# Optimization experiments

Hardware: AMD Instinct MI355X
Metric: run time of the kernel (lower is better)

## Reference

```python
import jax, jax.numpy as jnp
import numpy as np

B, S, D, H, V, N_SHARDS, CAP = 4, 512, 512, 8, 32000, 64, 128
HD = D // H


def _layernorm(x, g, b, eps=1e-5):
    mu = x.mean(-1, keepdims=True)
    var = ((x - mu) ** 2).mean(-1, keepdims=True)
    return (x - mu) * jax.lax.rsqrt(var + eps) * g + b


def setup_inputs() -> dict:
    key = jax.random.key(0)
    ks = jax.random.split(key, 16)
    s = 0.02
    return {
        'input_ids': jax.random.randint(ks[0], (B, S), 0, V, dtype=jnp.int32),
        'emb': jax.random.normal(ks[1], (V, D), jnp.float32) * s,
        'Wq': jax.random.normal(ks[2], (D, D), jnp.float32) * s,
        'Wk': jax.random.normal(ks[3], (D, D), jnp.float32) * s,
        'Wv': jax.random.normal(ks[4], (D, D), jnp.float32) * s,
        'Wo': jax.random.normal(ks[5], (D, D), jnp.float32) * s,
        'ln_g': jnp.ones((D,), jnp.float32),
        'ln_b': jnp.zeros((D,), jnp.float32),
        'W_router': jax.random.normal(ks[6], (D, N_SHARDS), jnp.float32),
        'mem_keys': jax.random.normal(ks[7], (N_SHARDS, CAP, D), jnp.float32) * s,
        'mem_values': jax.random.normal(ks[8], (N_SHARDS, CAP, D), jnp.float32) * s,
        'Wg_c': jax.random.normal(ks[9], (D, D), jnp.float32) * s,
        'Wg_m': jax.random.normal(ks[10], (D, D), jnp.float32) * s,
        'bg': jnp.zeros((D,), jnp.float32),
        'Wd': jax.random.normal(ks[11], (D, V), jnp.float32) * s,
        'bd': jnp.zeros((V,), jnp.float32),
        'top_k': 4,
    }


def reference(input_ids, emb, Wq, Wk, Wv, Wo, ln_g, ln_b, W_router,
              mem_keys, mem_values, Wg_c, Wg_m, bg, Wd, bd, top_k):
    # --- encode_context: embedding + causal MHA block (ContextSynthesizer) ---
    x = emb[input_ids]                                   # [B,S,D]
    q = (x @ Wq).reshape(B, S, H, HD)
    k = (x @ Wk).reshape(B, S, H, HD)
    v = (x @ Wv).reshape(B, S, H, HD)
    att = jnp.einsum('bqhd,bkhd->bhqk', q, k) / jnp.sqrt(jnp.float32(HD))
    causal = jnp.tril(jnp.ones((S, S), bool))
    att = jnp.where(causal[None, None], att, jnp.finfo(att.dtype).min)
    att = jax.nn.softmax(att, axis=-1)
    o = jnp.einsum('bhqk,bkhd->bqhd', att, v).reshape(B, S, D) @ Wo
    ctx = _layernorm(x + o, ln_g, ln_b)                  # [B,S,D]

    # --- LSHRouter: hyperplane projection -> shard id per token ---
    routes = jnp.argmax(ctx @ W_router, axis=-1)         # [B,S] int

    # --- MemoryShardStore.query, batched: per-token routed shard top-k read ---
    keys_g = mem_keys[routes]                            # [B,S,CAP,D] irregular gather
    scores = jnp.einsum('bscd,bsd->bsc', keys_g, ctx)    # [B,S,CAP]
    top_v, top_i = jax.lax.top_k(scores, top_k)          # [B,S,k]
    w = jax.nn.softmax(top_v, axis=-1)
    vals = mem_values[routes[:, :, None], top_i]         # [B,S,k,D]
    memory_stream = jnp.einsum('bsk,bskd->bsd', w, vals)

    # --- GatedMemoryFusion ---
    gate = jax.nn.sigmoid(ctx @ Wg_c + memory_stream @ Wg_m + bg)
    fused = gate * ctx + (1.0 - gate) * memory_stream

    # --- decoder; payload bias is zero (store holds no sequence_chunk records) ---
    logits = fused @ Wd + bd                             # [B,S,V]
    return logits
```

## Files before the change

kernel.cpp:

```cpp
#include <hip/hip_runtime.h>

typedef unsigned short u16;
typedef float f32x4 __attribute__((ext_vector_type(4)));
typedef short short8 __attribute__((ext_vector_type(8)));
typedef __bf16 bf16x8 __attribute__((ext_vector_type(8)));

#define B_  4
#define S_  512
#define D_  512
#define H_  8
#define HD_ 64
#define V_  32000
#define NSHARD_ 64
#define CAP_ 128
#define TOK_ (B_ * S_)

__device__ __forceinline__ float bf2f(u16 u) { return __uint_as_float(((unsigned)u) << 16); }
__device__ __forceinline__ u16 f2bf(float f) {
  unsigned u = __float_as_uint(f);
  u += 0x7FFFu + ((u >> 16) & 1u);
  return (u16)(u >> 16);
}

__device__ __forceinline__ f32x4 mfma16(short8 a, short8 b, f32x4 c) {
  return __builtin_amdgcn_mfma_f32_16x16x32_bf16(
      __builtin_bit_cast(bf16x8, a), __builtin_bit_cast(bf16x8, b), c, 0, 0, 0);
}

__device__ __forceinline__ void load_lds16(const void* g, void* l) {
  __builtin_amdgcn_global_load_lds(
      (const __attribute__((address_space(1))) void*)g,
      (__attribute__((address_space(3))) void*)l, 16, 0, 0);
}

template<int NS, bool ACC, int OM, bool CKLIM>
__global__ __launch_bounds__(256) void gemm_bt(
    const u16* __restrict__ Ah, const u16* __restrict__ Al, int ldA, long sA1, long sA2,
    const u16* __restrict__ Bh, const u16* __restrict__ Bl, int ldB, long sB1, long sB2,
    void* __restrict__ C0, void* __restrict__ C1, int ldC, long sC1, long sC2,
    int K, int z2n, float alpha)
{
  __shared__ u16 AsH[64 * 64];
  __shared__ u16 BsH[64 * 64];
  __shared__ u16 AsL[(NS == 3) ? 64 * 64 : 8];
  __shared__ u16 BsL[(NS == 3) ? 64 * 64 : 8];

  const int n0 = blockIdx.x * 64;
  const int m0 = blockIdx.y * 64;

  const int z = blockIdx.z;
  const int z1 = z / z2n, z2 = z - z1 * z2n;
  const long baseA = (long)z1 * sA1 + (long)z2 * sA2;
  const long baseB = (long)z1 * sB1 + (long)z2 * sB2;
  const long baseC = (long)z1 * sC1 + (long)z2 * sC2;

  const int tid = threadIdx.x;
  const int lane = tid & 63;
  const int w = tid >> 6;
  const int wm = (w >> 1) * 32, wn = (w & 1) * 32;
  const int fr = lane & 15, kg = lane >> 4;

  const int srow = lane >> 3;
  const int schunk = (lane & 7) ^ srow;

  const u16* gAh = Ah + baseA + (long)(m0 + w * 16 + srow) * ldA + schunk * 8;
  const u16* gBh = Bh + baseB + (long)(n0 + w * 16 + srow) * ldB + schunk * 8;
  const u16* gAl = (NS == 3) ? (Al + baseA + (long)(m0 + w * 16 + srow) * ldA + schunk * 8) : nullptr;
  const u16* gBl = (NS == 3) ? (Bl + baseB + (long)(n0 + w * 16 + srow) * ldB + schunk * 8) : nullptr;
  u16* lAh = &AsH[(w * 16) * 64];
  u16* lBh = &BsH[(w * 16) * 64];
  u16* lAl = &AsL[(NS == 3) ? (w * 16) * 64 : 0];
  u16* lBl = &BsL[(NS == 3) ? (w * 16) * 64 : 0];

  const int kmax = CKLIM ? (m0 + 64) : K;

  f32x4 acc[2][2] = {};

  for (int k0 = 0; k0 < kmax; k0 += 64) {
    load_lds16(gAh + k0, lAh);
    load_lds16(gAh + k0 + 8 * ldA, lAh + 8 * 64);
    load_lds16(gBh + k0, lBh);
    load_lds16(gBh + k0 + 8 * ldB, lBh + 8 * 64);
    if (NS == 3) {
      load_lds16(gAl + k0, lAl);
      load_lds16(gAl + k0 + 8 * ldA, lAl + 8 * 64);
      load_lds16(gBl + k0, lBl);
      load_lds16(gBl + k0 + 8 * ldB, lBl + 8 * 64);
    }
    __syncthreads();

    short8 ah[2][2], bh[2][2], al[2][2], bl[2][2];
#pragma unroll
    for (int mi = 0; mi < 2; ++mi) {
      int row = wm + mi * 16 + fr;
#pragma unroll
      for (int ks = 0; ks < 2; ++ks) {
        int idx = row * 64 + ((ks * 32 + kg * 8) ^ ((fr & 7) << 3));
        ah[mi][ks] = *(const short8*)&AsH[idx];
        if (NS == 3) al[mi][ks] = *(const short8*)&AsL[idx];
      }
    }
#pragma unroll
    for (int ni = 0; ni < 2; ++ni) {
      int row = wn + ni * 16 + fr;
#pragma unroll
      for (int ks = 0; ks < 2; ++ks) {
        int idx = row * 64 + ((ks * 32 + kg * 8) ^ ((fr & 7) << 3));
        bh[ni][ks] = *(const short8*)&BsH[idx];
        if (NS == 3) bl[ni][ks] = *(const short8*)&BsL[idx];
      }
    }
#pragma unroll
    for (int ks = 0; ks < 2; ++ks)
#pragma unroll
      for (int mi = 0; mi < 2; ++mi)
#pragma unroll
        for (int ni = 0; ni < 2; ++ni) {
          acc[mi][ni] = mfma16(ah[mi][ks], bh[ni][ks], acc[mi][ni]);
          if (NS == 3) {
            acc[mi][ni] = mfma16(ah[mi][ks], bl[ni][ks], acc[mi][ni]);
            acc[mi][ni] = mfma16(al[mi][ks], bh[ni][ks], acc[mi][ni]);
          }
        }
    __syncthreads();
  }

#pragma unroll
  for (int mi = 0; mi < 2; ++mi)
#pragma unroll
    for (int ni = 0; ni < 2; ++ni) {
      int gnc = n0 + wn + ni * 16 + fr;
#pragma unroll
      for (int r = 0; r < 4; ++r) {
        int gm = m0 + wm + mi * 16 + kg * 4 + r;
        float v = acc[mi][ni][r] * alpha;
        long idx = baseC + (long)gm * ldC + gnc;
        if (OM == 0) {
          float* C = (float*)C0;
          C[idx] = ACC ? (C[idx] + v) : v;
        } else {
          u16 h = f2bf(v);
          ((u16*)C0)[idx] = h;
          ((u16*)C1)[idx] = f2bf(v - bf2f(h));
        }
      }
    }
}

__global__ __launch_bounds__(256) void gate_gemm_k(
    const u16* __restrict__ Ah, const u16* __restrict__ Bh,
    const float* __restrict__ bgp, const float* __restrict__ ctxf,
    const float* __restrict__ msf, u16* __restrict__ fused)
{
  __shared__ u16 AsH[64 * 64];
  __shared__ u16 BsH[64 * 64];

  const int n0 = blockIdx.x * 64;
  const int m0 = blockIdx.y * 64;
  const int tid = threadIdx.x;
  const int lane = tid & 63;
  const int w = tid >> 6;
  const int wm = (w >> 1) * 32, wn = (w & 1) * 32;
  const int fr = lane & 15, kg = lane >> 4;
  const int srow = lane >> 3;
  const int schunk = (lane & 7) ^ srow;

  const u16* gAh = Ah + (long)(m0 + w * 16 + srow) * 1024 + schunk * 8;
  const u16* gBh = Bh + (long)(n0 + w * 16 + srow) * 1024 + schunk * 8;
  u16* lAh = &AsH[(w * 16) * 64];
  u16* lBh = &BsH[(w * 16) * 64];

  f32x4 acc[2][2] = {};

  for (int k0 = 0; k0 < 1024; k0 += 64) {
    load_lds16(gAh + k0, lAh);
    load_lds16(gAh + k0 + 8 * 1024, lAh + 8 * 64);
    load_lds16(gBh + k0, lBh);
    load_lds16(gBh + k0 + 8 * 1024, lBh + 8 * 64);
    __syncthreads();

    short8 ah[2][2], bh[2][2];
#pragma unroll
    for (int mi = 0; mi < 2; ++mi) {
      int row = wm + mi * 16 + fr;
#pragma unroll
      for (int ks = 0; ks < 2; ++ks)
        ah[mi][ks] = *(const short8*)&AsH[row * 64 +
                         ((ks * 32 + kg * 8) ^ ((fr & 7) << 3))];
    }
#pragma unroll
    for (int ni = 0; ni < 2; ++ni) {
      int row = wn + ni * 16 + fr;
#pragma unroll
      for (int ks = 0; ks < 2; ++ks)
        bh[ni][ks] = *(const short8*)&BsH[row * 64 +
                         ((ks * 32 + kg * 8) ^ ((fr & 7) << 3))];
    }
#pragma unroll
    for (int ks = 0; ks < 2; ++ks)
#pragma unroll
      for (int mi = 0; mi < 2; ++mi)
#pragma unroll
        for (int ni = 0; ni < 2; ++ni)
          acc[mi][ni] = mfma16(ah[mi][ks], bh[ni][ks], acc[mi][ni]);
    __syncthreads();
  }

#pragma unroll
  for (int mi = 0; mi < 2; ++mi)
#pragma unroll
    for (int ni = 0; ni < 2; ++ni) {
      int gnc = n0 + wn + ni * 16 + fr;
      float bv = bgp[gnc];
#pragma unroll
      for (int r = 0; r < 4; ++r) {
        int gm = m0 + wm + mi * 16 + kg * 4 + r;
        long idx = (long)gm * D_ + gnc;
        float g = 1.f / (1.f + expf(-(acc[mi][ni][r] + bv)));
        fused[idx] = f2bf(g * ctxf[idx] + (1.f - g) * msf[idx]);
      }
    }
}

__global__ __launch_bounds__(256) void qkt_k(
    const u16* __restrict__ qkvh, const u16* __restrict__ qkvl,
    float* __restrict__ att)
{
  const int n0 = blockIdx.x * 64;
  const int m0 = blockIdx.y * 64;
  if (n0 > m0 + 63) return;
  const int z = blockIdx.z;
  const int b = z >> 3, h = z & 7;
  const long qbase = (long)b * 512 * 1536 + h * 64;
  const long kbase = qbase + 512;
  const long cbase = (long)z * 512 * 512;

  const int tid = threadIdx.x;
  const int lane = tid & 63;
  const int w = tid >> 6;
  const int wm = (w >> 1) * 32, wn = (w & 1) * 32;
  const int fr = lane & 15, kg = lane >> 4;

  short8 ah[2][2], al[2][2], bh[2][2], bl[2][2];
#pragma unroll
  for (int mi = 0; mi < 2; ++mi)
#pragma unroll
    for (int ks = 0; ks < 2; ++ks) {
      long ra = qbase + (long)(m0 + wm + mi * 16 + fr) * 1536 + ks * 32 + kg * 8;
      ah[mi][ks] = *(const short8*)(qkvh + ra);
      al[mi][ks] = *(const short8*)(qkvl + ra);
    }
#pragma unroll
  for (int ni = 0; ni < 2; ++ni)
#pragma unroll
    for (int ks = 0; ks < 2; ++ks) {
      long rb = kbase + (long)(n0 + wn + ni * 16 + fr) * 1536 + ks * 32 + kg * 8;
      bh[ni][ks] = *(const short8*)(qkvh + rb);
      bl[ni][ks] = *(const short8*)(qkvl + rb);
    }

  f32x4 acc[2][2] = {};
#pragma unroll
  for (int ks = 0; ks < 2; ++ks)
#pragma unroll
    for (int mi = 0; mi < 2; ++mi)
#pragma unroll
      for (int ni = 0; ni < 2; ++ni) {
        acc[mi][ni] = mfma16(ah[mi][ks], bh[ni][ks], acc[mi][ni]);
        acc[mi][ni] = mfma16(ah[mi][ks], bl[ni][ks], acc[mi][ni]);
        acc[mi][ni] = mfma16(al[mi][ks], bh[ni][ks], acc[mi][ni]);
      }

#pragma unroll
  for (int mi = 0; mi < 2; ++mi)
#pragma unroll
    for (int ni = 0; ni < 2; ++ni) {
      int gnc = n0 + wn + ni * 16 + fr;
#pragma unroll
      for (int r = 0; r < 4; ++r) {
        int gm = m0 + wm + mi * 16 + kg * 4 + r;
        att[cbase + (long)gm * 512 + gnc] = acc[mi][ni][r] * 0.125f;
      }
    }
}

__global__ __launch_bounds__(512, 4) void logits_gemm_bk32_k(
    const u16* __restrict__ A, const u16* __restrict__ Bt,
    const float* __restrict__ bias, float* __restrict__ C)
{
  __shared__ u16 As[2][256 * 32];
  __shared__ u16 Bs[2][128 * 32];

  const int id = blockIdx.x;
  const int swz = (id & 7) * 250 + (id >> 3);
  const int m0 = (swz & 7) * 256;
  const int n0 = (swz >> 3) * 128;

  const int tid = threadIdx.x;
  const int lane = tid & 63;
  const int wid = tid >> 6;
  const int wr = wid >> 1;
  const int wc = wid & 1;
  const int fr = lane & 15, kg = lane >> 4;
  const int srow = lane >> 2;
  const int schunk = (lane & 3) ^ (srow & 3);

  f32x4 acc[4][4] = {};
  short8 a[4], b[4];

  auto stage = [&](int kt) {
    const int buf = kt & 1;
    const long kc = (long)kt * 32 + schunk * 8;
    load_lds16(A + (long)(m0 + wid * 16 + srow) * D_ + kc,
               &As[buf][(wid * 16) * 32]);
    load_lds16(A + (long)(m0 + 128 + wid * 16 + srow) * D_ + kc,
               &As[buf][(128 + wid * 16) * 32]);
    load_lds16(Bt + (long)(n0 + wid * 16 + srow) * D_ + kc,
               &Bs[buf][(wid * 16) * 32]);
  };
  auto readfrags = [&](int buf) {
#pragma unroll
    for (int mi = 0; mi < 4; ++mi) {
      int row = wr * 64 + mi * 16 + fr;
      a[mi] = *(const short8*)&As[buf][row * 32 + ((kg ^ (row & 3)) * 8)];
    }
#pragma unroll
    for (int ni = 0; ni < 4; ++ni) {
      int row = wc * 64 + ni * 16 + fr;
      b[ni] = *(const short8*)&Bs[buf][row * 32 + ((kg ^ (row & 3)) * 8)];
    }
  };

  stage(0);
  stage(1);

  for (int t = 0; t < 16; ++t) {
    __builtin_amdgcn_sched_barrier(0);
    if (t < 15) { asm volatile("s_waitcnt vmcnt(3)" ::: "memory"); }
    else        { asm volatile("s_waitcnt vmcnt(0)" ::: "memory"); }
    __builtin_amdgcn_s_barrier();
    __builtin_amdgcn_sched_barrier(0);

    readfrags(t & 1);
    asm volatile("s_waitcnt lgkmcnt(0)" ::: "memory");
    __builtin_amdgcn_sched_barrier(0);
    __builtin_amdgcn_s_barrier();
    __builtin_amdgcn_sched_barrier(0);

    if (t + 2 < 16) stage(t + 2);

    __builtin_amdgcn_sched_barrier(0);
    __builtin_amdgcn_s_setprio(1);
#pragma unroll
    for (int mi = 0; mi < 4; ++mi)
#pragma unroll
      for (int ni = 0; ni < 4; ++ni)
        acc[mi][ni] = mfma16(a[mi], b[ni], acc[mi][ni]);
    __builtin_amdgcn_s_setprio(0);
    __builtin_amdgcn_sched_barrier(0);
  }

#pragma unroll
  for (int ni = 0; ni < 4; ++ni) {
    int gnc = n0 + wc * 64 + ni * 16 + fr;
    float bv = bias[gnc];
#pragma unroll
    for (int mi = 0; mi < 4; ++mi)
#pragma unroll
      for (int r = 0; r < 4; ++r) {
        int gm = m0 + wr * 64 + mi * 16 + kg * 4 + r;
        __builtin_nontemporal_store(acc[mi][ni][r] + bv, &C[(long)gm * V_ + gnc]);
      }
  }
}

__global__ __launch_bounds__(256) void prep_weights_k(
    const float* __restrict__ Wq, const float* __restrict__ Wk,
    const float* __restrict__ Wv, const float* __restrict__ Wo,
    const float* __restrict__ Wgc, const float* __restrict__ Wgm,
    const float* __restrict__ Wd,
    u16* __restrict__ wqkvTh, u16* __restrict__ wqkvTl,
    u16* __restrict__ woTh, u16* __restrict__ woTl,
    u16* __restrict__ wgT, u16* __restrict__ wdT)
{
  const int bid = blockIdx.x;
  const float* W; u16 *oh, *ol = nullptr;
  int ldw, ldo, koff = 0, nb, kb;
  bool LO = false;
  if (bid < 384) {
    const int w = bid >> 6, tt = bid & 63;
    nb = tt & 7; kb = tt >> 3;
    ldw = 512; ldo = 512;
    switch (w) {
      case 0: W = Wq;  oh = wqkvTh;               ol = wqkvTl;               LO = true; break;
      case 1: W = Wk;  oh = wqkvTh + 512 * 512;   ol = wqkvTl + 512 * 512;   LO = true; break;
      case 2: W = Wv;  oh = wqkvTh + 2 * 512 * 512; ol = wqkvTl + 2 * 512 * 512; LO = true; break;
      case 3: W = Wo;  oh = woTh;                 ol = woTl;                 LO = true; break;
      case 4: W = Wgc; oh = wgT; ldo = 1024; break;
      default: W = Wgm; oh = wgT; ldo = 1024; koff = 512; break;
    }
  } else {
    const int tt = bid - 384;
    nb = tt % 500; kb = tt / 500;
    W = Wd; ldw = V_; ldo = 512; oh = wdT;
  }
  const int n0 = nb * 64, k0 = kb * 64;
  const int tid = threadIdx.x;
  __shared__ float t[64][65];
  {
    const int kk = tid >> 4;
    const int c4 = (tid & 15) * 4;
#pragma unroll
    for (int i = 0; i < 4; ++i) {
      f32x4 v = *(const f32x4*)(W + (long)(k0 + kk + i * 16) * ldw + n0 + c4);
      t[kk + i * 16][c4] = v[0];
      t[kk + i * 16][c4 + 1] = v[1];
      t[kk + i * 16][c4 + 2] = v[2];
      t[kk + i * 16][c4 + 3] = v[3];
    }
  }
  __syncthreads();
  {
    const int chunk = tid & 7;
    const int nn = tid >> 3;
#pragma unroll
    for (int j = 0; j < 2; ++j) {
      int n = nn + j * 32;
      u16 hbuf[8], lbuf[8];
#pragma unroll
      for (int e = 0; e < 8; ++e) {
        float fv = t[chunk * 8 + e][n];
        u16 h = f2bf(fv);
        hbuf[e] = h;
        lbuf[e] = f2bf(fv - bf2f(h));
      }
      long ob = (long)(n0 + n) * ldo + koff + k0 + chunk * 8;
      *(short8*)(oh + ob) = *(short8*)hbuf;
      if (LO) *(short8*)(ol + ob) = *(short8*)lbuf;
    }
  }
}

__global__ __launch_bounds__(256) void v_transpose_k(
    const u16* __restrict__ qh, const u16* __restrict__ ql,
    u16* __restrict__ vTh, u16* __restrict__ vTl)
{
  __shared__ u16 th[64][68];
  __shared__ u16 tl[64][68];
  const int z = blockIdx.y;
  const int b = z >> 3, h = z & 7;
  const int s0 = blockIdx.x * 64;
  const long ibase = ((long)(b * 512 + s0)) * 1536 + 1024 + h * 64;
  const int tid = threadIdx.x;
  {
    const int sr = tid >> 2;
    const int c8 = (tid & 3) * 16;
    const long src = ibase + (long)sr * 1536 + c8;
    *(short8*)&th[sr][c8]     = *(const short8*)(qh + src);
    *(short8*)&th[sr][c8 + 8] = *(const short8*)(qh + src + 8);
    *(short8*)&tl[sr][c8]     = *(const short8*)(ql + src);
    *(short8*)&tl[sr][c8 + 8] = *(const short8*)(ql + src + 8);
  }
  __syncthreads();
  {
    const int dr = tid >> 2;
    const int s8 = (tid & 3) * 16;
    u16 oh[16], ol[16];
#pragma unroll
    for (int j = 0; j < 16; ++j) { oh[j] = th[s8 + j][dr]; ol[j] = tl[s8 + j][dr]; }
    long ob = (long)z * 64 * 512 + (long)dr * 512 + s0 + s8;
    *(short8*)(vTh + ob)     = *(short8*)&oh[0];
    *(short8*)(vTh + ob + 8) = *(short8*)&oh[8];
    *(short8*)(vTl + ob)     = *(short8*)&ol[0];
    *(short8*)(vTl + ob + 8) = *(short8*)&ol[8];
  }
}

__global__ __launch_bounds__(128) void embed_k(const int* __restrict__ ids,
                                               const float* __restrict__ emb,
                                               float* __restrict__ x,
                                               u16* __restrict__ xh,
                                               u16* __restrict__ xl) {
  const int t = blockIdx.x;
  const long id = ids[t];
  const int c = threadIdx.x * 4;
  f32x4 v = *(const f32x4*)(emb + id * (long)D_ + c);
  *(f32x4*)(x + (long)t * D_ + c) = v;
  u16 hh[4], ll[4];
#pragma unroll
  for (int j = 0; j < 4; ++j) {
    u16 h = f2bf(v[j]);
    hh[j] = h;
    ll[j] = f2bf(v[j] - bf2f(h));
  }
  *(unsigned long long*)(xh + (long)t * D_ + c) = *(unsigned long long*)hh;
  *(unsigned long long*)(xl + (long)t * D_ + c) = *(unsigned long long*)ll;
}

__global__ __launch_bounds__(64) void softmax_causal_k(
    const float* __restrict__ att, u16* __restrict__ ph, u16* __restrict__ pl) {
  const int row = blockIdx.x;
  const int i = row & 511;
  const long base = (long)row << 9;
  const float* p = att + base;
  const int lane = threadIdx.x;
  const int c0 = lane * 8;
  float v[8];
  float m = -3.4e38f;
  if (c0 <= i) {
    f32x4 a = *(const f32x4*)(p + c0);
    f32x4 b2 = *(const f32x4*)(p + c0 + 4);
#pragma unroll
    for (int j = 0; j < 8; ++j) {
      float x = (j < 4) ? a[j] : b2[j - 4];
      x = (c0 + j <= i) ? x : -3.4e38f;
      v[j] = x;
      m = fmaxf(m, x);
    }
  } else {
#pragma unroll
    for (int j = 0; j < 8; ++j) v[j] = 0.f;
  }
#pragma unroll
  for (int off = 32; off; off >>= 1) m = fmaxf(m, __shfl_xor(m, off));
  float s = 0.f;
  if (c0 <= i) {
#pragma unroll
    for (int j = 0; j < 8; ++j) {
      float e = (c0 + j <= i) ? expf(v[j] - m) : 0.f;
      v[j] = e;
      s += e;
    }
  }
#pragma unroll
  for (int off = 32; off; off >>= 1) s += __shfl_xor(s, off);
  float inv = 1.f / s;
  if (c0 <= (i | 63)) {
    u16 hh[8], ll[8];
#pragma unroll
    for (int j = 0; j < 8; ++j) {
      float e = (c0 <= i) ? v[j] * inv : 0.f;
      u16 h = f2bf(e);
      hh[j] = h;
      ll[j] = f2bf(e - bf2f(h));
    }
    *(short8*)(ph + base + c0) = *(short8*)hh;
    *(short8*)(pl + base + c0) = *(short8*)ll;
  }
}

__global__ __launch_bounds__(128) void ln_route_k(
    const float* __restrict__ x, const float* __restrict__ proj,
    const float* __restrict__ g, const float* __restrict__ b,
    const float* __restrict__ Wr, const float* __restrict__ keys,
    const float* __restrict__ valsm,
    float* __restrict__ ctxf, u16* __restrict__ catA, float* __restrict__ msf)
{
  const int t = blockIdx.x;
  const int tid = threadIdx.x;
  __shared__ float sctx[D_];
  __shared__ float red2[4];
  __shared__ float spart[CAP_];
  __shared__ float sred2[2][64];
  __shared__ int s_route;
  __shared__ int sidx[4];
  __shared__ float sw[4];

  const int c = tid * 4;
  f32x4 xv = *(const f32x4*)(x + (long)t * D_ + c);
  f32x4 pv = *(const f32x4*)(proj + (long)t * D_ + c);
  float v0 = xv[0] + pv[0], v1 = xv[1] + pv[1];
  float v2 = xv[2] + pv[2], v3 = xv[3] + pv[3];
  float s = v0 + v1 + v2 + v3;
  float q = v0 * v0 + v1 * v1 + v2 * v2 + v3 * v3;
#pragma unroll
  for (int off = 32; off; off >>= 1) { s += __shfl_xor(s, off); q += __shfl_xor(q, off); }
  const int wave = tid >> 6, lane = tid & 63;
  if (lane == 0) { red2[wave] = s; red2[2 + wave] = q; }
  __syncthreads();
  s = red2[0] + red2[1];
  q = red2[2] + red2[3];
  float mu = s * (1.f / 512.f);
  float var = q * (1.f / 512.f) - mu * mu;
  float rs = rsqrtf(var + 1e-5f);
  f32x4 gv = *(const f32x4*)(g + c);
  f32x4 bv = *(const f32x4*)(b + c);
  f32x4 of;
  of[0] = (v0 - mu) * rs * gv[0] + bv[0];
  of[1] = (v1 - mu) * rs * gv[1] + bv[1];
  of[2] = (v2 - mu) * rs * gv[2] + bv[2];
  of[3] = (v3 - mu) * rs * gv[3] + bv[3];
  *(f32x4*)(ctxf + (long)t * D_ + c) = of;
  ((f32x4*)sctx)[tid] = of;
  {
    u16 hh[4];
#pragma unroll
    for (int j = 0; j < 4; ++j) hh[j] = f2bf(of[j]);
    *(unsigned long long*)(catA + (long)t * 1024 + c) = *(unsigned long long*)hh;
  }
  __syncthreads();

  {
    const int cc = tid & 63, half = tid >> 6;
    float accr = 0.f;
    const float* cp = sctx + half * 256;
    const float* wp = Wr + (long)(half * 256) * NSHARD_ + cc;
    for (int d = 0; d < 256; ++d) accr += cp[d] * wp[(long)d * NSHARD_];
    sred2[half][cc] = accr;
  }
  __syncthreads();
  if (tid < 64) {
    float v = sred2[0][tid] + sred2[1][tid];
    int idx = tid;
#pragma unroll
    for (int off = 32; off; off >>= 1) {
      float ov = __shfl_xor(v, off);
      int oi = __shfl_xor(idx, off);
      if (ov > v || (ov == v && oi < idx)) { v = ov; idx = oi; }
    }
    if (tid == 0) s_route = idx;
  }
  __syncthreads();
  const int route = s_route;

  {
    const float* krow = keys + ((long)route * CAP_ + tid) * D_;
    float sc = 0.f;
    for (int d0 = 0; d0 < D_; d0 += 4) {
      f32x4 kv = *(const f32x4*)(krow + d0);
      sc += sctx[d0] * kv[0] + sctx[d0 + 1] * kv[1] +
            sctx[d0 + 2] * kv[2] + sctx[d0 + 3] * kv[3];
    }
    spart[tid] = sc;
  }
  __syncthreads();

  for (int rep = 0; rep < 4; ++rep) {
    if (tid < 64) {
      float v1r = spart[tid]; int i1 = tid;
      float v2r = spart[tid + 64]; int i2 = tid + 64;
      float v; int idx;
      if (v2r > v1r) { v = v2r; idx = i2; } else { v = v1r; idx = i1; }
#pragma unroll
      for (int off = 32; off; off >>= 1) {
        float ov = __shfl_xor(v, off);
        int oi = __shfl_xor(idx, off);
        if (ov > v || (ov == v && oi < idx)) { v = ov; idx = oi; }
      }
      if (tid == 0) { sidx[rep] = idx; sw[rep] = v; spart[idx] = -3.4e38f; }
    }
    __syncthreads();
  }

  float w0 = sw[0], w1 = sw[1], w2 = sw[2], w3 = sw[3];
  float mx = fmaxf(fmaxf(w0, w1), fmaxf(w2, w3));
  float e0 = expf(w0 - mx), e1 = expf(w1 - mx), e2 = expf(w2 - mx), e3 = expf(w3 - mx);
  float inv = 1.f / (e0 + e1 + e2 + e3);
  float wk[4] = {e0 * inv, e1 * inv, e2 * inv, e3 * inv};

  float a0 = 0, a1 = 0, a2 = 0, a3 = 0;
#pragma unroll
  for (int k = 0; k < 4; ++k) {
    const float* vr = valsm + ((long)route * CAP_ + sidx[k]) * D_ + c;
    f32x4 vv = *(const f32x4*)vr;
    float w = wk[k];
    a0 += w * vv[0]; a1 += w * vv[1]; a2 += w * vv[2]; a3 += w * vv[3];
  }
  f32x4 om; om[0] = a0; om[1] = a1; om[2] = a2; om[3] = a3;
  *(f32x4*)(msf + (long)t * D_ + c) = om;
  u16 oh[4];
  oh[0] = f2bf(a0); oh[1] = f2bf(a1); oh[2] = f2bf(a2); oh[3] = f2bf(a3);
  *(unsigned long long*)(catA + (long)t * 1024 + 512 + c) =
      *(unsigned long long*)oh;
}

extern "C" void kernel_launch(void* const* d_in, const int* in_sizes, int n_in,
                              void* d_out, int out_size, void* d_ws, size_t ws_size,
                              hipStream_t stream) {
  const int*   ids  = (const int*)d_in[0];
  const float* emb  = (const float*)d_in[1];
  const float* Wq   = (const float*)d_in[2];
  const float* Wk   = (const float*)d_in[3];
  const float* Wv   = (const float*)d_in[4];
  const float* Wo   = (const float*)d_in[5];
  const float* ln_g = (const float*)d_in[6];
  const float* ln_b = (const float*)d_in[7];
  const float* Wr   = (const float*)d_in[8];
  const float* mk   = (const float*)d_in[9];
  const float* mv   = (const float*)d_in[10];
  const float* Wgc  = (const float*)d_in[11];
  const float* Wgm  = (const float*)d_in[12];
  const float* bg   = (const float*)d_in[13];
  const float* Wd   = (const float*)d_in[14];
  const float* bd   = (const float*)d_in[15];
  float* out = (float*)d_out;

  char* ws = (char*)d_ws;
  size_t off = 0;
  auto alloc = [&](size_t bytes) -> void* {
    void* p = ws + off;
    off += (bytes + 255) & ~(size_t)255;
    return p;
  };
  float* x      = (float*)alloc((size_t)TOK_ * D_ * 4);
  u16*   xh     = (u16*)  alloc((size_t)TOK_ * D_ * 2);
  u16*   xl     = (u16*)  alloc((size_t)TOK_ * D_ * 2);
  u16*   wqkvTh = (u16*)  alloc((size_t)3 * D_ * D_ * 2);
  u16*   wqkvTl = (u16*)  alloc((size_t)3 * D_ * D_ * 2);
  u16*   woTh   = (u16*)  alloc((size_t)D_ * D_ * 2);
  u16*   woTl   = (u16*)  alloc((size_t)D_ * D_ * 2);
  u16*   wgT    = (u16*)  alloc((size_t)D_ * 1024 * 2);
  u16*   wdT    = (u16*)  alloc((size_t)D_ * V_ * 2);
  u16*   qkvh   = (u16*)  alloc((size_t)TOK_ * 3 * D_ * 2);
  u16*   qkvl   = (u16*)  alloc((size_t)TOK_ * 3 * D_ * 2);
  u16*   vTh    = (u16*)  alloc((size_t)B_ * H_ * HD_ * S_ * 2);
  u16*   vTl    = (u16*)  alloc((size_t)B_ * H_ * HD_ * S_ * 2);
  float* att    = (float*)alloc((size_t)B_ * H_ * S_ * S_ * 4);
  u16*   ph     = (u16*)  alloc((size_t)B_ * H_ * S_ * S_ * 2);
  u16*   pl     = (u16*)  alloc((size_t)B_ * H_ * S_ * S_ * 2);
  u16*   oh     = (u16*)  alloc((size_t)TOK_ * D_ * 2);
  u16*   ol     = (u16*)  alloc((size_t)TOK_ * D_ * 2);
  float* proj   = (float*)alloc((size_t)TOK_ * D_ * 4);
  float* ctxf   = (float*)alloc((size_t)TOK_ * D_ * 4);
  u16*   catA   = (u16*)  alloc((size_t)TOK_ * 1024 * 2);
  float* msf    = (float*)alloc((size_t)TOK_ * D_ * 4);
  u16*   fused  = (u16*)  alloc((size_t)TOK_ * D_ * 2);

  prep_weights_k<<<4384, 256, 0, stream>>>(
      Wq, Wk, Wv, Wo, Wgc, Wgm, Wd,
      wqkvTh, wqkvTl, woTh, woTl, wgT, wdT);

  embed_k<<<TOK_, 128, 0, stream>>>(ids, emb, x, xh, xl);

  {
    dim3 g(1536 / 64, TOK_ / 64, 1);
    gemm_bt<3, false, 1, false><<<g, 256, 0, stream>>>(
        xh, xl, D_, 0, 0, wqkvTh, wqkvTl, D_, 0, 0,
        qkvh, qkvl, 1536, 0, 0, D_, 1, 1.f);
  }

  {
    dim3 g(S_ / 64, B_ * H_, 1);
    v_transpose_k<<<g, 256, 0, stream>>>(qkvh, qkvl, vTh, vTl);
  }

  {
    dim3 g(S_ / 64, S_ / 64, B_ * H_);
    qkt_k<<<g, 256, 0, stream>>>(qkvh, qkvl, att);
  }

  softmax_causal_k<<<B_ * H_ * S_, 64, 0, stream>>>(att, ph, pl);

  {
    dim3 g(1, S_ / 64, B_ * H_);
    gemm_bt<3, false, 1, true><<<g, 256, 0, stream>>>(
        ph, pl, S_, (long)H_ * S_ * S_, (long)S_ * S_,
        vTh, vTl, S_, (long)H_ * HD_ * S_, (long)HD_ * S_,
        oh, ol, D_, (long)S_ * D_, HD_,
        S_, H_, 1.f);
  }

  {
    dim3 g(D_ / 64, TOK_ / 64, 1);
    gemm_bt<3, false, 0, false><<<g, 256, 0, stream>>>(
        oh, ol, D_, 0, 0, woTh, woTl, D_, 0, 0,
        proj, nullptr, D_, 0, 0, D_, 1, 1.f);
  }

  ln_route_k<<<TOK_, 128, 0, stream>>>(
      x, proj, ln_g, ln_b, Wr, mk, mv, ctxf, catA, msf);

  {
    dim3 g(D_ / 64, TOK_ / 64, 1);
    gate_gemm_k<<<g, 256, 0, stream>>>(catA, wgT, bg, ctxf, msf, fused);
  }

  logits_gemm_bk32_k<<<2000, 512, 0, stream>>>(fused, wdT, bd, out);
}
```

Measured before the change: 299.3 us.

## Fuse causal QK^T, softmax and PV into a flash-style attention kernel

Replaces the three-kernel attention (QK^T to an fp32 score buffer, causal softmax writing split bf16 probabilities, then a batched PV GEMM) with one online-softmax kernel per 64-row query block and head. Probabilities stay in LDS as hi/lo bf16 pairs, so the large B*H*S*S score and probability buffers and their global traffic disappear. The generic GEMM loses its batching, accumulate and causal-limit template options because they are no longer used. The trade-off is only 256 blocks, each walking a causal number of key blocks, so the load is unbalanced and K/V are read straight from global memory without LDS staging.

```diff
diff --git a/kernel.cpp b/kernel.cpp
--- a/kernel.cpp
+++ b/kernel.cpp
@@ -33,12 +33,12 @@
       (__attribute__((address_space(3))) void*)l, 16, 0, 0);
 }
 
-template<int NS, bool ACC, int OM, bool CKLIM>
+template<int NS, int OM>
 __global__ __launch_bounds__(256) void gemm_bt(
-    const u16* __restrict__ Ah, const u16* __restrict__ Al, int ldA, long sA1, long sA2,
-    const u16* __restrict__ Bh, const u16* __restrict__ Bl, int ldB, long sB1, long sB2,
-    void* __restrict__ C0, void* __restrict__ C1, int ldC, long sC1, long sC2,
-    int K, int z2n, float alpha)
+    const u16* __restrict__ Ah, const u16* __restrict__ Al, int ldA,
+    const u16* __restrict__ Bh, const u16* __restrict__ Bl, int ldB,
+    void* __restrict__ C0, void* __restrict__ C1, int ldC,
+    int K)
 {
   __shared__ u16 AsH[64 * 64];
   __shared__ u16 BsH[64 * 64];
@@ -48,12 +48,6 @@
   const int n0 = blockIdx.x * 64;
   const int m0 = blockIdx.y * 64;
 
-  const int z = blockIdx.z;
-  const int z1 = z / z2n, z2 = z - z1 * z2n;
-  const long baseA = (long)z1 * sA1 + (long)z2 * sA2;
-  const long baseB = (long)z1 * sB1 + (long)z2 * sB2;
-  const long baseC = (long)z1 * sC1 + (long)z2 * sC2;
-
   const int tid = threadIdx.x;
   const int lane = tid & 63;
   const int w = tid >> 6;
@@ -63,20 +57,18 @@
   const int srow = lane >> 3;
   const int schunk = (lane & 7) ^ srow;
 
-  const u16* gAh = Ah + baseA + (long)(m0 + w * 16 + srow) * ldA + schunk * 8;
-  const u16* gBh = Bh + baseB + (long)(n0 + w * 16 + srow) * ldB + schunk * 8;
-  const u16* gAl = (NS == 3) ? (Al + baseA + (long)(m0 + w * 16 + srow) * ldA + schunk * 8) : nullptr;
-  const u16* gBl = (NS == 3) ? (Bl + baseB + (long)(n0 + w * 16 + srow) * ldB + schunk * 8) : nullptr;
+  const u16* gAh = Ah + (long)(m0 + w * 16 + srow) * ldA + schunk * 8;
+  const u16* gBh = Bh + (long)(n0 + w * 16 + srow) * ldB + schunk * 8;
+  const u16* gAl = (NS == 3) ? (Al + (long)(m0 + w * 16 + srow) * ldA + schunk * 8) : nullptr;
+  const u16* gBl = (NS == 3) ? (Bl + (long)(n0 + w * 16 + srow) * ldB + schunk * 8) : nullptr;
   u16* lAh = &AsH[(w * 16) * 64];
   u16* lBh = &BsH[(w * 16) * 64];
   u16* lAl = &AsL[(NS == 3) ? (w * 16) * 64 : 0];
   u16* lBl = &BsL[(NS == 3) ? (w * 16) * 64 : 0];
 
-  const int kmax = CKLIM ? (m0 + 64) : K;
-
   f32x4 acc[2][2] = {};
 
-  for (int k0 = 0; k0 < kmax; k0 += 64) {
+  for (int k0 = 0; k0 < K; k0 += 64) {
     load_lds16(gAh + k0, lAh);
     load_lds16(gAh + k0 + 8 * ldA, lAh + 8 * 64);
     load_lds16(gBh + k0, lBh);
@@ -133,17 +125,146 @@
 #pragma unroll
       for (int r = 0; r < 4; ++r) {
         int gm = m0 + wm + mi * 16 + kg * 4 + r;
-        float v = acc[mi][ni][r] * alpha;
-        long idx = baseC + (long)gm * ldC + gnc;
+        float v = acc[mi][ni][r];
+        long idx = (long)gm * ldC + gnc;
         if (OM == 0) {
-          float* C = (float*)C0;
-          C[idx] = ACC ? (C[idx] + v) : v;
+          ((float*)C0)[idx] = v;
         } else {
           u16 h = f2bf(v);
           ((u16*)C0)[idx] = h;
           ((u16*)C1)[idx] = f2bf(v - bf2f(h));
         }
       }
+    }
+}
+
+__global__ __launch_bounds__(256) void attn_k(
+    const u16* __restrict__ qkvh, const u16* __restrict__ qkvl,
+    const u16* __restrict__ vTh, const u16* __restrict__ vTl,
+    u16* __restrict__ oh, u16* __restrict__ ol)
+{
+  const int mb = blockIdx.x;
+  const int z = blockIdx.y;
+  const int b = z >> 3, h = z & 7;
+  const int m0 = mb * 64;
+  const long qbase = (long)b * 512 * 1536 + h * 64;
+  const long kbase = qbase + 512;
+  const long vbase = (long)z * 64 * 512;
+
+  const int tid = threadIdx.x;
+  const int lane = tid & 63;
+  const int w = tid >> 6;
+  const int fr = lane & 15, kg = lane >> 4;
+
+  __shared__ u16 p_h[4][16 * 64];
+  __shared__ u16 p_l[4][16 * 64];
+
+  short8 qh_[2], ql_[2];
+#pragma unroll
+  for (int ks = 0; ks < 2; ++ks) {
+    long ra = qbase + (long)(m0 + w * 16 + fr) * 1536 + ks * 32 + kg * 8;
+    qh_[ks] = *(const short8*)(qkvh + ra);
+    ql_[ks] = *(const short8*)(qkvl + ra);
+  }
+
+  f32x4 acc_o[4] = {};
+  float m_run[4], l_run[4];
+#pragma unroll
+  for (int r = 0; r < 4; ++r) { m_run[r] = -3.4e38f; l_run[r] = 0.f; }
+
+  for (int kb = 0; kb <= mb; ++kb) {
+    f32x4 s4[4] = {};
+#pragma unroll
+    for (int ks = 0; ks < 2; ++ks)
+#pragma unroll
+      for (int ni = 0; ni < 4; ++ni) {
+        long rb = kbase + (long)(kb * 64 + ni * 16 + fr) * 1536 + ks * 32 + kg * 8;
+        short8 kh = *(const short8*)(qkvh + rb);
+        short8 kl = *(const short8*)(qkvl + rb);
+        s4[ni] = mfma16(qh_[ks], kh, s4[ni]);
+        s4[ni] = mfma16(qh_[ks], kl, s4[ni]);
+        s4[ni] = mfma16(ql_[ks], kh, s4[ni]);
+      }
+    float tmax[4];
+#pragma unroll
+    for (int r = 0; r < 4; ++r) tmax[r] = -3.4e38f;
+#pragma unroll
+    for (int ni = 0; ni < 4; ++ni)
+#pragma unroll
+      for (int r = 0; r < 4; ++r) {
+        int row = m0 + w * 16 + kg * 4 + r;
+        int col = kb * 64 + ni * 16 + fr;
+        float sv = (col <= row) ? s4[ni][r] * 0.125f : -3.4e38f;
+        s4[ni][r] = sv;
+        tmax[r] = fmaxf(tmax[r], sv);
+      }
+#pragma unroll
+    for (int r = 0; r < 4; ++r)
+#pragma unroll
+      for (int off = 8; off; off >>= 1)
+        tmax[r] = fmaxf(tmax[r], __shfl_xor(tmax[r], off));
+
+    float tsum[4];
+#pragma unroll
+    for (int r = 0; r < 4; ++r) {
+      float mn = fmaxf(m_run[r], tmax[r]);
+      float sc = expf(m_run[r] - mn);
+      m_run[r] = mn;
+      l_run[r] *= sc;
+#pragma unroll
+      for (int ni = 0; ni < 4; ++ni) acc_o[ni][r] *= sc;
+      tsum[r] = 0.f;
+    }
+
+    __syncthreads();
+#pragma unroll
+    for (int ni = 0; ni < 4; ++ni)
+#pragma unroll
+      for (int r = 0; r < 4; ++r) {
+        float p = expf(s4[ni][r] - m_run[r]);
+        tsum[r] += p;
+        int rl = kg * 4 + r;
+        int chunk = (ni * 2 + (fr >> 3)) ^ (rl & 7);
+        int addr = rl * 64 + chunk * 8 + (fr & 7);
+        u16 hv = f2bf(p);
+        p_h[w][addr] = hv;
+        p_l[w][addr] = f2bf(p - bf2f(hv));
+      }
+#pragma unroll
+    for (int r = 0; r < 4; ++r) {
+#pragma unroll
+      for (int off = 8; off; off >>= 1) tsum[r] += __shfl_xor(tsum[r], off);
+      l_run[r] += tsum[r];
+    }
+    __syncthreads();
+
+#pragma unroll
+    for (int ks = 0; ks < 2; ++ks) {
+      int ca = fr * 64 + (((ks * 4 + kg) ^ (fr & 7)) * 8);
+      short8 pah = *(const short8*)&p_h[w][ca];
+      short8 pal = *(const short8*)&p_l[w][ca];
+#pragma unroll
+      for (int ni = 0; ni < 4; ++ni) {
+        long rv = vbase + (long)(ni * 16 + fr) * 512 + kb * 64 + ks * 32 + kg * 8;
+        short8 vh = *(const short8*)(vTh + rv);
+        short8 vl = *(const short8*)(vTl + rv);
+        acc_o[ni] = mfma16(pah, vh, acc_o[ni]);
+        acc_o[ni] = mfma16(pah, vl, acc_o[ni]);
+        acc_o[ni] = mfma16(pal, vh, acc_o[ni]);
+      }
+    }
+  }
+
+#pragma unroll
+  for (int ni = 0; ni < 4; ++ni)
+#pragma unroll
+    for (int r = 0; r < 4; ++r) {
+      float ov = acc_o[ni][r] / l_run[r];
+      long orow = (long)(b * 512 + m0 + w * 16 + kg * 4 + r);
+      long oidx = orow * 512 + h * 64 + ni * 16 + fr;
+      u16 hv = f2bf(ov);
+      oh[oidx] = hv;
+      ol[oidx] = f2bf(ov - bf2f(hv));
     }
 }
 
@@ -218,68 +339,6 @@
         long idx = (long)gm * D_ + gnc;
         float g = 1.f / (1.f + expf(-(acc[mi][ni][r] + bv)));
         fused[idx] = f2bf(g * ctxf[idx] + (1.f - g) * msf[idx]);
-      }
-    }
-}
-
-__global__ __launch_bounds__(256) void qkt_k(
-    const u16* __restrict__ qkvh, const u16* __restrict__ qkvl,
-    float* __restrict__ att)
-{
-  const int n0 = blockIdx.x * 64;
-  const int m0 = blockIdx.y * 64;
-  if (n0 > m0 + 63) return;
-  const int z = blockIdx.z;
-  const int b = z >> 3, h = z & 7;
-  const long qbase = (long)b * 512 * 1536 + h * 64;
-  const long kbase = qbase + 512;
-  const long cbase = (long)z * 512 * 512;
-
-  const int tid = threadIdx.x;
-  const int lane = tid & 63;
-  const int w = tid >> 6;
-  const int wm = (w >> 1) * 32, wn = (w & 1) * 32;
-  const int fr = lane & 15, kg = lane >> 4;
-
-  short8 ah[2][2], al[2][2], bh[2][2], bl[2][2];
-#pragma unroll
-  for (int mi = 0; mi < 2; ++mi)
-#pragma unroll
-    for (int ks = 0; ks < 2; ++ks) {
-      long ra = qbase + (long)(m0 + wm + mi * 16 + fr) * 1536 + ks * 32 + kg * 8;
-      ah[mi][ks] = *(const short8*)(qkvh + ra);
-      al[mi][ks] = *(const short8*)(qkvl + ra);
-    }
-#pragma unroll
-  for (int ni = 0; ni < 2; ++ni)
-#pragma unroll
-    for (int ks = 0; ks < 2; ++ks) {
-      long rb = kbase + (long)(n0 + wn + ni * 16 + fr) * 1536 + ks * 32 + kg * 8;
-      bh[ni][ks] = *(const short8*)(qkvh + rb);
-      bl[ni][ks] = *(const short8*)(qkvl + rb);
-    }
-
-  f32x4 acc[2][2] = {};
-#pragma unroll
-  for (int ks = 0; ks < 2; ++ks)
-#pragma unroll
-    for (int mi = 0; mi < 2; ++mi)
-#pragma unroll
-      for (int ni = 0; ni < 2; ++ni) {
-        acc[mi][ni] = mfma16(ah[mi][ks], bh[ni][ks], acc[mi][ni]);
-        acc[mi][ni] = mfma16(ah[mi][ks], bl[ni][ks], acc[mi][ni]);
-        acc[mi][ni] = mfma16(al[mi][ks], bh[ni][ks], acc[mi][ni]);
-      }
-
-#pragma unroll
-  for (int mi = 0; mi < 2; ++mi)
-#pragma unroll
-    for (int ni = 0; ni < 2; ++ni) {
-      int gnc = n0 + wn + ni * 16 + fr;
-#pragma unroll
-      for (int r = 0; r < 4; ++r) {
-        int gm = m0 + wm + mi * 16 + kg * 4 + r;
-        att[cbase + (long)gm * 512 + gnc] = acc[mi][ni][r] * 0.125f;
       }
     }
 }
@@ -497,58 +556,6 @@
   *(unsigned long long*)(xl + (long)t * D_ + c) = *(unsigned long long*)ll;
 }
 
-__global__ __launch_bounds__(64) void softmax_causal_k(
-    const float* __restrict__ att, u16* __restrict__ ph, u16* __restrict__ pl) {
-  const int row = blockIdx.x;
-  const int i = row & 511;
-  const long base = (long)row << 9;
-  const float* p = att + base;
-  const int lane = threadIdx.x;
-  const int c0 = lane * 8;
-  float v[8];
-  float m = -3.4e38f;
-  if (c0 <= i) {
-    f32x4 a = *(const f32x4*)(p + c0);
-    f32x4 b2 = *(const f32x4*)(p + c0 + 4);
-#pragma unroll
-    for (int j = 0; j < 8; ++j) {
-      float x = (j < 4) ? a[j] : b2[j - 4];
-      x = (c0 + j <= i) ? x : -3.4e38f;
-      v[j] = x;
-      m = fmaxf(m, x);
-    }
-  } else {
-#pragma unroll
-    for (int j = 0; j < 8; ++j) v[j] = 0.f;
-  }
-#pragma unroll
-  for (int off = 32; off; off >>= 1) m = fmaxf(m, __shfl_xor(m, off));
-  float s = 0.f;
-  if (c0 <= i) {
-#pragma unroll
-    for (int j = 0; j < 8; ++j) {
-      float e = (c0 + j <= i) ? expf(v[j] - m) : 0.f;
-      v[j] = e;
-      s += e;
-    }
-  }
-#pragma unroll
-  for (int off = 32; off; off >>= 1) s += __shfl_xor(s, off);
-  float inv = 1.f / s;
-  if (c0 <= (i | 63)) {
-    u16 hh[8], ll[8];
-#pragma unroll
-    for (int j = 0; j < 8; ++j) {
-      float e = (c0 <= i) ? v[j] * inv : 0.f;
-      u16 h = f2bf(e);
-      hh[j] = h;
-      ll[j] = f2bf(e - bf2f(h));
-    }
-    *(short8*)(ph + base + c0) = *(short8*)hh;
-    *(short8*)(pl + base + c0) = *(short8*)ll;
-  }
-}
-
 __global__ __launch_bounds__(128) void ln_route_k(
     const float* __restrict__ x, const float* __restrict__ proj,
     const float* __restrict__ g, const float* __restrict__ b,
@@ -668,10 +675,10 @@
   }
   f32x4 om; om[0] = a0; om[1] = a1; om[2] = a2; om[3] = a3;
   *(f32x4*)(msf + (long)t * D_ + c) = om;
-  u16 oh[4];
-  oh[0] = f2bf(a0); oh[1] = f2bf(a1); oh[2] = f2bf(a2); oh[3] = f2bf(a3);
+  u16 ohh[4];
+  ohh[0] = f2bf(a0); ohh[1] = f2bf(a1); ohh[2] = f2bf(a2); ohh[3] = f2bf(a3);
   *(unsigned long long*)(catA + (long)t * 1024 + 512 + c) =
-      *(unsigned long long*)oh;
+      *(unsigned long long*)ohh;
 }
 
 extern "C" void kernel_launch(void* const* d_in, const int* in_sizes, int n_in,
@@ -715,9 +722,6 @@
   u16*   qkvl   = (u16*)  alloc((size_t)TOK_ * 3 * D_ * 2);
   u16*   vTh    = (u16*)  alloc((size_t)B_ * H_ * HD_ * S_ * 2);
   u16*   vTl    = (u16*)  alloc((size_t)B_ * H_ * HD_ * S_ * 2);
-  float* att    = (float*)alloc((size_t)B_ * H_ * S_ * S_ * 4);
-  u16*   ph     = (u16*)  alloc((size_t)B_ * H_ * S_ * S_ * 2);
-  u16*   pl     = (u16*)  alloc((size_t)B_ * H_ * S_ * S_ * 2);
   u16*   oh     = (u16*)  alloc((size_t)TOK_ * D_ * 2);
   u16*   ol     = (u16*)  alloc((size_t)TOK_ * D_ * 2);
   float* proj   = (float*)alloc((size_t)TOK_ * D_ * 4);
@@ -734,9 +738,8 @@
 
   {
     dim3 g(1536 / 64, TOK_ / 64, 1);
-    gemm_bt<3, false, 1, false><<<g, 256, 0, stream>>>(
-        xh, xl, D_, 0, 0, wqkvTh, wqkvTl, D_, 0, 0,
-        qkvh, qkvl, 1536, 0, 0, D_, 1, 1.f);
+    gemm_bt<3, 1><<<g, 256, 0, stream>>>(
+        xh, xl, D_, wqkvTh, wqkvTl, D_, qkvh, qkvl, 1536, D_);
   }
 
   {
@@ -745,26 +748,14 @@
   }
 
   {
-    dim3 g(S_ / 64, S_ / 64, B_ * H_);
-    qkt_k<<<g, 256, 0, stream>>>(qkvh, qkvl, att);
-  }
-
-  softmax_causal_k<<<B_ * H_ * S_, 64, 0, stream>>>(att, ph, pl);
-
-  {
-    dim3 g(1, S_ / 64, B_ * H_);
-    gemm_bt<3, false, 1, true><<<g, 256, 0, stream>>>(
-        ph, pl, S_, (long)H_ * S_ * S_, (long)S_ * S_,
-        vTh, vTl, S_, (long)H_ * HD_ * S_, (long)HD_ * S_,
-        oh, ol, D_, (long)S_ * D_, HD_,
-        S_, H_, 1.f);
+    dim3 g(S_ / 64, B_ * H_, 1);
+    attn_k<<<g, 256, 0, stream>>>(qkvh, qkvl, vTh, vTl, oh, ol);
   }
 
   {
     dim3 g(D_ / 64, TOK_ / 64, 1);
-    gemm_bt<3, false, 0, false><<<g, 256, 0, stream>>>(
-        oh, ol, D_, 0, 0, woTh, woTl, D_, 0, 0,
-        proj, nullptr, D_, 0, 0, D_, 1, 1.f);
+    gemm_bt<3, 0><<<g, 256, 0, stream>>>(
+        oh, ol, D_, woTh, woTl, D_, proj, nullptr, D_, D_);
   }
 
   ln_route_k<<<TOK_, 128, 0, stream>>>(
```

After: 306.8 us. 2.5% more time.
